# Kernel tuning notes

Hardware: AMD Instinct MI355X
Metric: run time of the kernel (lower is better)

## Reference

```python
import jax, jax.numpy as jnp
import numpy as np

U, I, D, K, B, NNEG = 500000, 500000, 64, 32, 8192, 128
W1, W2, W3, W4 = 1e-6, 1.0, 1e-6, 1.0
NEG_WEIGHT, GAMMA, LAMBDA = 200.0, 1e-4, 2.5


def setup_inputs() -> dict:
    key = jax.random.key(0)
    ks = jax.random.split(key, 14)
    return {
        "users": jax.random.randint(ks[0], (B,), 0, U),
        "pos_items": jax.random.randint(ks[1], (B,), 0, I),
        "neg_items": jax.random.randint(ks[2], (B, NNEG), 0, I),
        "rpkms": jax.random.normal(ks[3], (B,), dtype=jnp.float32),
        "user_emb": jax.random.normal(ks[4], (U, D), dtype=jnp.float32) * 1e-2,
        "item_emb": jax.random.normal(ks[5], (I, D), dtype=jnp.float32) * 1e-2,
        "beta_uD": jax.random.uniform(ks[6], (U,), dtype=jnp.float32),
        "beta_iD": jax.random.uniform(ks[7], (I,), dtype=jnp.float32),
        "ii_neighbor_mat": jax.random.randint(ks[8], (I, K), 0, I),
        "ii_constraint_mat": jax.random.uniform(ks[9], (I, K), dtype=jnp.float32),
        "mse_u_w": jax.random.normal(ks[10], (D, D), dtype=jnp.float32) * 0.05,
        "mse_u_b": jnp.zeros((D,), jnp.float32),
        "mse_i_w": jax.random.normal(ks[11], (D, D), dtype=jnp.float32) * 0.05,
        "mse_i_b": jnp.zeros((D,), jnp.float32),
        "fc1_w1": jax.random.normal(ks[12], (D, 2 * D), dtype=jnp.float32) * 0.05,
        "fc1_b1": jnp.zeros((D,), jnp.float32),
        "fc1_w2": jax.random.normal(ks[13], (1, D), dtype=jnp.float32) * 0.05,
        "fc1_b2": jnp.zeros((1,), jnp.float32),
    }


def reference(users, pos_items, neg_items, rpkms, user_emb, item_emb,
              beta_uD, beta_iD, ii_neighbor_mat, ii_constraint_mat,
              mse_u_w, mse_u_b, mse_i_w, mse_i_b,
              fc1_w1, fc1_b1, fc1_w2, fc1_b2):
    sp = jax.nn.softplus  # -log(sigmoid(x)) == softplus(-x)

    ue = user_emb[users]            # [B, D]
    pe = item_emb[pos_items]        # [B, D]
    ne = item_emb[neg_items]        # [B, N, D]

    # ---- omegas ----
    pos_w = W1 + W2 * beta_uD[users] * beta_iD[pos_items]          # [B]
    neg_w = W3 + W4 * beta_uD[users][:, None] * beta_iD[neg_items]  # [B, N]

    # ---- cal_loss_L (weighted BCE with logits) ----
    pos_scores = jnp.sum(ue * pe, axis=-1)                  # [B]
    neg_scores = jnp.einsum('bd,bnd->bn', ue, ne)           # [B, N]
    pos_loss = pos_w * sp(-pos_scores)                      # label 1
    neg_loss = jnp.mean(neg_w * sp(neg_scores), axis=-1)    # label 0, mean over negs
    loss_L = jnp.mean(pos_loss + neg_loss * NEG_WEIGHT)

    # ---- norm_loss over all learned parameters ----
    params = (user_emb, item_emb, mse_u_w, mse_u_b, mse_i_w, mse_i_b,
              fc1_w1, fc1_b1, fc1_w2, fc1_b2)
    norm = GAMMA * 0.5 * sum(jnp.sum(p * p) for p in params)

    # ---- cal_loss_I: gather item-item neighbors of pos_items ----
    nbr = item_emb[ii_neighbor_mat[pos_items]]              # [B, K, D]
    sim = ii_constraint_mat[pos_items]                      # [B, K]
    loss_I = LAMBDA * jnp.mean(sim * sp(-jnp.einsum('bd,bkd->bk', ue, nbr)))

    # ---- mse_loss ----
    feat_u = ue @ mse_u_w.T + mse_u_b
    feat_i = pe @ mse_i_w.T + mse_i_b
    pred = jnp.sum(feat_u * feat_i, axis=-1)
    mse = jnp.mean((pred - rpkms) ** 2)

    total = loss_L + norm + loss_I + mse
    zero = jnp.float32(0.0)  # torch returns torch.tensor(0.0) as 4th element
    return jnp.stack([total, loss_L, loss_I, zero, mse, norm])
```

## Files before the change

kernel.cpp:

```cpp
#include <hip/hip_runtime.h>
#include <math.h>

#define UU 500000
#define II 500000
#define DD 64
#define KK 32
#define BB 8192
#define NNEG 128

typedef float v4f __attribute__((ext_vector_type(4)));

__device__ __forceinline__ float softplus_f(float x) {
    return fmaxf(x, 0.0f) + log1pf(expf(-fabsf(x)));
}

__device__ __forceinline__ float waveReduceSum(float v) {
#pragma unroll
    for (int off = 32; off > 0; off >>= 1) v += __shfl_xor(v, off, 64);
    return v;
}

__device__ __forceinline__ unsigned int bf16pack2(float lo, float hi) {
    unsigned int ul = __float_as_uint(lo);
    ul += 0x7FFFu + ((ul >> 16) & 1u);
    unsigned int uh = __float_as_uint(hi);
    uh += 0x7FFFu + ((uh >> 16) & 1u);
    return (ul >> 16) | (uh & 0xFFFF0000u);
}

__global__ __launch_bounds__(256) void norm_convert_kernel(
    const float* __restrict__ user_emb, const float* __restrict__ item_emb,
    unsigned int* __restrict__ bfit,
    const float* __restrict__ mse_u_w, const float* __restrict__ mse_u_b,
    const float* __restrict__ mse_i_w, const float* __restrict__ mse_i_b,
    const float* __restrict__ fc1_w1, const float* __restrict__ fc1_b1,
    const float* __restrict__ fc1_w2, const float* __restrict__ fc1_b2,
    float* __restrict__ acc)
{
    const size_t tid = (size_t)blockIdx.x * blockDim.x + threadIdx.x;
    const size_t st  = (size_t)gridDim.x * blockDim.x;
    float s = 0.f;

    {
        const size_t npair = (size_t)II * DD / 8;
        const v4f* it4 = (const v4f*)item_emb;
        uint4* out4 = (uint4*)bfit;
        for (size_t k = tid; k < npair; k += st) {
            v4f a = __builtin_nontemporal_load(&it4[2 * k]);
            v4f b = __builtin_nontemporal_load(&it4[2 * k + 1]);
            s += a.x*a.x + a.y*a.y + a.z*a.z + a.w*a.w;
            s += b.x*b.x + b.y*b.y + b.z*b.z + b.w*b.w;
            uint4 w;
            w.x = bf16pack2(a.x, a.y);
            w.y = bf16pack2(a.z, a.w);
            w.z = bf16pack2(b.x, b.y);
            w.w = bf16pack2(b.z, b.w);
            out4[k] = w;
        }
    }
    {
        const size_t n4 = (size_t)UU * DD / 4;
        const v4f* a = (const v4f*)user_emb;
        for (size_t i = tid; i < n4; i += st) {
            v4f x = __builtin_nontemporal_load(&a[i]);
            s += x.x*x.x + x.y*x.y + x.z*x.z + x.w*x.w;
        }
    }
    for (size_t i = tid; i < (size_t)DD * DD; i += st)
        s += mse_u_w[i] * mse_u_w[i] + mse_i_w[i] * mse_i_w[i];
    for (size_t i = tid; i < (size_t)DD * 2 * DD; i += st)
        s += fc1_w1[i] * fc1_w1[i];
    for (size_t i = tid; i < (size_t)DD; i += st)
        s += mse_u_b[i] * mse_u_b[i] + mse_i_b[i] * mse_i_b[i]
           + fc1_b1[i] * fc1_b1[i] + fc1_w2[i] * fc1_w2[i];
    if (tid == 0) s += fc1_b2[0] * fc1_b2[0];

    s = waveReduceSum(s);
    __shared__ float red[4];
    if ((threadIdx.x & 63) == 0) red[threadIdx.x >> 6] = s;
    __syncthreads();
    if (threadIdx.x == 0)
        atomicAdd(&acc[2], red[0] + red[1] + red[2] + red[3]);
}

__global__ __launch_bounds__(256) void gather_mse_kernel(
    const int* __restrict__ users, const int* __restrict__ pos_items,
    const int* __restrict__ neg_items, const float* __restrict__ rpkms,
    const float* __restrict__ user_emb, const float* __restrict__ item_emb,
    const unsigned int* __restrict__ bfit,
    const float* __restrict__ beta_uD, const float* __restrict__ beta_iD,
    const int* __restrict__ ii_nbr, const float* __restrict__ ii_con,
    const float* __restrict__ mse_u_w, const float* __restrict__ mse_u_b,
    const float* __restrict__ mse_i_w, const float* __restrict__ mse_i_b,
    float* __restrict__ acc)
{
    const int wave = threadIdx.x >> 6;
    const int lane = threadIdx.x & 63;
    const int b = blockIdx.x * 4 + wave;

    const int u_idx = users[b];
    const int p_idx = pos_items[b];
    const float u_reg = user_emb[(size_t)u_idx * DD + lane];
    const float p_reg = item_emb[(size_t)p_idx * DD + lane];
    const float bu = beta_uD[u_idx];

    __shared__ float sU[4][DD];
    __shared__ float sP[4][DD];
    sU[wave][lane] = u_reg;
    sP[wave][lane] = p_reg;

    const int q  = lane & 3;
    const int li = lane >> 2;

    float4 uv[4], pv[4];
#pragma unroll
    for (int j = 0; j < 4; ++j) {
        uv[j] = *(const float4*)&sU[wave][q * 16 + j * 4];
        pv[j] = *(const float4*)&sP[wave][q * 16 + j * 4];
    }

    float accL = 0.f, accI = 0.f, accM = 0.f;

    {
        const float pos_dot = waveReduceSum(u_reg * p_reg);
        if (lane == 0)
            accL += (1e-6f + bu * beta_iD[p_idx]) * softplus_f(-pos_dot);
    }

    const int i0 = neg_items[(size_t)b * NNEG + lane];
    const int i1 = neg_items[(size_t)b * NNEG + 64 + lane];
    const float bn0 = beta_iD[i0];
    const float bn1 = beta_iD[i1];
    int nbv = 0; float simv = 0.f;
    if (lane < KK) {
        nbv  = ii_nbr[(size_t)p_idx * KK + lane];
        simv = ii_con[(size_t)p_idx * KK + lane];
    }

    const float negscale4 = 0.25f * (200.0f / (float)NNEG);

    uint4 rg[3][2];
    float rw[3];

#define PREP(g, slot)                                                          \
    {                                                                          \
        int idx; float w;                                                      \
        if ((g) < 4)      { idx = __shfl(i0, (g) * 16 + li, 64);               \
                            w   = __shfl(bn0, (g) * 16 + li, 64); }            \
        else if ((g) < 8) { idx = __shfl(i1, ((g) - 4) * 16 + li, 64);         \
                            w   = __shfl(bn1, ((g) - 4) * 16 + li, 64); }      \
        else              { idx = __shfl(nbv, ((g) - 8) * 16 + li, 64);        \
                            w   = __shfl(simv, ((g) - 8) * 16 + li, 64); }     \
        const uint4* row = (const uint4*)(bfit + (size_t)idx * (DD / 2));      \
        rg[slot][0] = row[q * 2];                                              \
        rg[slot][1] = row[q * 2 + 1];                                          \
        rw[slot] = w;                                                          \
    }

#define DOT8(wv, ua, ub, d)                                                    \
    {                                                                          \
        d = fmaf(__uint_as_float((wv).x << 16), ua.x, d);                      \
        d = fmaf(__uint_as_float((wv).x & 0xFFFF0000u), ua.y, d);              \
        d = fmaf(__uint_as_float((wv).y << 16), ua.z, d);                      \
        d = fmaf(__uint_as_float((wv).y & 0xFFFF0000u), ua.w, d);              \
        d = fmaf(__uint_as_float((wv).z << 16), ub.x, d);                      \
        d = fmaf(__uint_as_float((wv).z & 0xFFFF0000u), ub.y, d);              \
        d = fmaf(__uint_as_float((wv).w << 16), ub.z, d);                      \
        d = fmaf(__uint_as_float((wv).w & 0xFFFF0000u), ub.w, d);              \
    }

#define CONSUME(g, slot)                                                       \
    {                                                                          \
        float dot = 0.f;                                                       \
        DOT8(rg[slot][0], uv[0], uv[1], dot);                                  \
        DOT8(rg[slot][1], uv[2], uv[3], dot);                                  \
        dot += __shfl_xor(dot, 1, 64);                                         \
        dot += __shfl_xor(dot, 2, 64);                                         \
        if ((g) < 8) accL += negscale4 * (1e-6f + bu * rw[slot]) * softplus_f(dot); \
        else         accI += 0.25f * rw[slot] * softplus_f(-dot);              \
    }

    PREP(0, 0); PREP(1, 1); PREP(2, 2);
    CONSUME(0, 0); PREP(3, 0);
    CONSUME(1, 1); PREP(4, 1);
    CONSUME(2, 2); PREP(5, 2);
    CONSUME(3, 0); PREP(6, 0);
    CONSUME(4, 1); PREP(7, 1);
    CONSUME(5, 2); PREP(8, 2);
    CONSUME(6, 0); PREP(9, 0);
    CONSUME(7, 1);
    CONSUME(8, 2);
    CONSUME(9, 0);
#undef PREP
#undef DOT8
#undef CONSUME

    {
        float pq = 0.f;
#pragma unroll
        for (int g = 0; g < 4; ++g) {
            const int r = g * 16 + li;
            const float* wur = mse_u_w + r * DD + q * 16;
            const float* wir = mse_i_w + r * DD + q * 16;
            float fu = 0.f, fi = 0.f;
#pragma unroll
            for (int j = 0; j < 4; ++j) {
                const float4 a = *(const float4*)(wur + j * 4);
                fu = fmaf(a.x, uv[j].x, fu); fu = fmaf(a.y, uv[j].y, fu);
                fu = fmaf(a.z, uv[j].z, fu); fu = fmaf(a.w, uv[j].w, fu);
                const float4 c = *(const float4*)(wir + j * 4);
                fi = fmaf(c.x, pv[j].x, fi); fi = fmaf(c.y, pv[j].y, fi);
                fi = fmaf(c.z, pv[j].z, fi); fi = fmaf(c.w, pv[j].w, fi);
            }
            fu += __shfl_xor(fu, 1, 64); fu += __shfl_xor(fu, 2, 64);
            fi += __shfl_xor(fi, 1, 64); fi += __shfl_xor(fi, 2, 64);
            fu += mse_u_b[r];
            fi += mse_i_b[r];
            pq += fu * fi;
        }
        const float pred = waveReduceSum(pq) * 0.25f;
        if (lane == 0) {
            const float diff = pred - rpkms[b];
            accM += diff * diff;
        }
    }

    accL = waveReduceSum(accL);
    accI = waveReduceSum(accI);
    __shared__ float redL[4], redI[4], redM[4];
    if (lane == 0) { redL[wave] = accL; redI[wave] = accI; redM[wave] = accM; }
    __syncthreads();
    if (threadIdx.x == 0) {
        atomicAdd(&acc[0], redL[0] + redL[1] + redL[2] + redL[3]);
        atomicAdd(&acc[1], redI[0] + redI[1] + redI[2] + redI[3]);
        atomicAdd(&acc[3], redM[0] + redM[1] + redM[2] + redM[3]);
    }
}

#define NORMB 1024
__global__ __launch_bounds__(256) void fb_fused_kernel(
    const int* __restrict__ users, const int* __restrict__ pos_items,
    const int* __restrict__ neg_items,
    const float* __restrict__ user_emb, const float* __restrict__ item_emb,
    const float* __restrict__ beta_uD, const float* __restrict__ beta_iD,
    const int* __restrict__ ii_nbr, const float* __restrict__ ii_con,
    const float* __restrict__ mse_u_w, const float* __restrict__ mse_u_b,
    const float* __restrict__ mse_i_w, const float* __restrict__ mse_i_b,
    const float* __restrict__ fc1_w1, const float* __restrict__ fc1_b1,
    const float* __restrict__ fc1_w2, const float* __restrict__ fc1_b2,
    float* __restrict__ acc)
{
    const int wave = threadIdx.x >> 6;
    const int lane = threadIdx.x & 63;
    __shared__ float red[4];

    if (blockIdx.x < NORMB) {
        const size_t tid = (size_t)blockIdx.x * blockDim.x + threadIdx.x;
        const size_t st  = (size_t)NORMB * 256;
        const size_t n4  = (size_t)UU * DD / 4;
        float s = 0.f;
        const v4f* a = (const v4f*)user_emb;
        for (size_t i = tid; i < n4; i += st) {
            v4f x = a[i]; s += x.x*x.x + x.y*x.y + x.z*x.z + x.w*x.w;
        }
        const v4f* c = (const v4f*)item_emb;
        for (size_t i = tid; i < n4; i += st) {
            v4f x = c[i]; s += x.x*x.x + x.y*x.y + x.z*x.z + x.w*x.w;
        }
        for (size_t i = tid; i < (size_t)DD * DD; i += st)
            s += mse_u_w[i] * mse_u_w[i] + mse_i_w[i] * mse_i_w[i];
        for (size_t i = tid; i < (size_t)DD * 2 * DD; i += st)
            s += fc1_w1[i] * fc1_w1[i];
        for (size_t i = tid; i < (size_t)DD; i += st)
            s += mse_u_b[i] * mse_u_b[i] + mse_i_b[i] * mse_i_b[i]
               + fc1_b1[i] * fc1_b1[i] + fc1_w2[i] * fc1_w2[i];
        if (tid == 0) s += fc1_b2[0] * fc1_b2[0];
        s = waveReduceSum(s);
        if (lane == 0) red[wave] = s;
        __syncthreads();
        if (threadIdx.x == 0)
            atomicAdd(&acc[2], red[0] + red[1] + red[2] + red[3]);
        return;
    }

    const int b = (blockIdx.x - NORMB) * 4 + wave;
    float accL = 0.f, accI = 0.f;
    const int u_idx = users[b];
    const int p_idx = pos_items[b];
    const float u_reg = user_emb[(size_t)u_idx * DD + lane];
    const float bu = beta_uD[u_idx];
    __shared__ float sU[4][DD];
    sU[wave][lane] = u_reg;
    const int q  = lane & 3;
    const int li = lane >> 2;
    float4 uv[4];
#pragma unroll
    for (int j = 0; j < 4; ++j) uv[j] = *(const float4*)&sU[wave][j * 16 + q * 4];
    {
        const float p = item_emb[(size_t)p_idx * DD + lane];
        const float pos_dot = waveReduceSum(u_reg * p);
        if (lane == 0) accL += (1e-6f + bu * beta_iD[p_idx]) * softplus_f(-pos_dot);
    }
    const int i0 = neg_items[(size_t)b * NNEG + lane];
    const int i1 = neg_items[(size_t)b * NNEG + 64 + lane];
    const float bn0 = beta_iD[i0];
    const float bn1 = beta_iD[i1];
    const float negscale4 = 0.25f * (200.0f / (float)NNEG);
#pragma unroll
    for (int g = 0; g < 2; ++g) {
        const int   srcI = g ? i1 : i0;
        const float srcB = g ? bn1 : bn0;
        float4 vb[4][4]; float bi4[4];
#pragma unroll
        for (int t = 0; t < 4; ++t) {
            const int n = t * 16 + li;
            const int idx = __shfl(srcI, n, 64);
            bi4[t] = __shfl(srcB, n, 64);
            const float* row = item_emb + (size_t)idx * DD + q * 4;
#pragma unroll
            for (int j = 0; j < 4; ++j) vb[t][j] = *(const float4*)(row + j * 16);
        }
#pragma unroll
        for (int t = 0; t < 4; ++t) {
            float dot = 0.f;
#pragma unroll
            for (int j = 0; j < 4; ++j) {
                dot = fmaf(vb[t][j].x, uv[j].x, dot);
                dot = fmaf(vb[t][j].y, uv[j].y, dot);
                dot = fmaf(vb[t][j].z, uv[j].z, dot);
                dot = fmaf(vb[t][j].w, uv[j].w, dot);
            }
            dot += __shfl_xor(dot, 1, 64);
            dot += __shfl_xor(dot, 2, 64);
            accL += negscale4 * (1e-6f + bu * bi4[t]) * softplus_f(dot);
        }
    }
    int nbv = 0; float simv = 0.f;
    if (lane < KK) {
        nbv  = ii_nbr[(size_t)p_idx * KK + lane];
        simv = ii_con[(size_t)p_idx * KK + lane];
    }
    {
        float4 vb[2][4]; float sk2[2];
#pragma unroll
        for (int t = 0; t < 2; ++t) {
            const int n = t * 16 + li;
            const int idx = __shfl(nbv, n, 64);
            sk2[t] = __shfl(simv, n, 64);
            const float* row = item_emb + (size_t)idx * DD + q * 4;
#pragma unroll
            for (int j = 0; j < 4; ++j) vb[t][j] = *(const float4*)(row + j * 16);
        }
#pragma unroll
        for (int t = 0; t < 2; ++t) {
            float dot = 0.f;
#pragma unroll
            for (int j = 0; j < 4; ++j) {
                dot = fmaf(vb[t][j].x, uv[j].x, dot);
                dot = fmaf(vb[t][j].y, uv[j].y, dot);
                dot = fmaf(vb[t][j].z, uv[j].z, dot);
                dot = fmaf(vb[t][j].w, uv[j].w, dot);
            }
            dot += __shfl_xor(dot, 1, 64);
            dot += __shfl_xor(dot, 2, 64);
            accI += 0.25f * sk2[t] * softplus_f(-dot);
        }
    }
    accL = waveReduceSum(accL);
    accI = waveReduceSum(accI);
    __shared__ float redL[4], redI[4];
    if (lane == 0) { redL[wave] = accL; redI[wave] = accI; }
    __syncthreads();
    if (threadIdx.x == 0) {
        atomicAdd(&acc[0], redL[0] + redL[1] + redL[2] + redL[3]);
        atomicAdd(&acc[1], redI[0] + redI[1] + redI[2] + redI[3]);
    }
}

__global__ __launch_bounds__(256) void fb_mse_kernel(
    const int* __restrict__ users, const int* __restrict__ pos_items,
    const float* __restrict__ rpkms,
    const float* __restrict__ user_emb, const float* __restrict__ item_emb,
    const float* __restrict__ mse_u_w, const float* __restrict__ mse_u_b,
    const float* __restrict__ mse_i_w, const float* __restrict__ mse_i_b,
    float* __restrict__ acc)
{
    __shared__ float sWu[DD * (DD + 1)];
    __shared__ float sWi[DD * (DD + 1)];
    __shared__ float sBu[DD], sBi[DD];
    __shared__ float sUe[4][DD], sPe[4][DD];
    for (int i = threadIdx.x; i < DD * DD; i += blockDim.x) {
        const int r = i >> 6, c = i & 63;
        sWu[r * (DD + 1) + c] = mse_u_w[i];
        sWi[r * (DD + 1) + c] = mse_i_w[i];
    }
    if (threadIdx.x < DD) {
        sBu[threadIdx.x] = mse_u_b[threadIdx.x];
        sBi[threadIdx.x] = mse_i_b[threadIdx.x];
    }
    const int wave = threadIdx.x >> 6;
    const int lane = threadIdx.x & 63;
    const int b = blockIdx.x * 4 + wave;
    sUe[wave][lane] = user_emb[(size_t)users[b] * DD + lane];
    sPe[wave][lane] = item_emb[(size_t)pos_items[b] * DD + lane];
    __syncthreads();
    float fu = sBu[lane];
    float fi = sBi[lane];
#pragma unroll 8
    for (int d = 0; d < DD; ++d) {
        fu += sUe[wave][d] * sWu[lane * (DD + 1) + d];
        fi += sPe[wave][d] * sWi[lane * (DD + 1) + d];
    }
    const float pred = waveReduceSum(fu * fi);
    if (lane == 0) {
        const float diff = pred - rpkms[b];
        atomicAdd(&acc[3], diff * diff);
    }
}

__global__ void finalize_kernel(const float* __restrict__ acc, float* __restrict__ out)
{
    if (threadIdx.x == 0) {
        const float loss_L = acc[0] / (float)BB;
        const float loss_I = 2.5f * acc[1] / (float)(BB * KK);
        const float mse    = acc[3] / (float)BB;
        const float norm   = 1e-4f * 0.5f * acc[2];
        const float total  = loss_L + norm + loss_I + mse;
        out[0] = total;
        out[1] = loss_L;
        out[2] = loss_I;
        out[3] = 0.0f;
        out[4] = mse;
        out[5] = norm;
    }
}

extern "C" void kernel_launch(void* const* d_in, const int* in_sizes, int n_in,
                              void* d_out, int out_size, void* d_ws, size_t ws_size,
                              hipStream_t stream)
{
    const int*   users      = (const int*)  d_in[0];
    const int*   pos_items  = (const int*)  d_in[1];
    const int*   neg_items  = (const int*)  d_in[2];
    const float* rpkms      = (const float*)d_in[3];
    const float* user_emb   = (const float*)d_in[4];
    const float* item_emb   = (const float*)d_in[5];
    const float* beta_uD    = (const float*)d_in[6];
    const float* beta_iD    = (const float*)d_in[7];
    const int*   ii_nbr     = (const int*)  d_in[8];
    const float* ii_con     = (const float*)d_in[9];
    const float* mse_u_w    = (const float*)d_in[10];
    const float* mse_u_b    = (const float*)d_in[11];
    const float* mse_i_w    = (const float*)d_in[12];
    const float* mse_i_b    = (const float*)d_in[13];
    const float* fc1_w1     = (const float*)d_in[14];
    const float* fc1_b1     = (const float*)d_in[15];
    const float* fc1_w2     = (const float*)d_in[16];
    const float* fc1_b2     = (const float*)d_in[17];

    float* acc = (float*)d_ws;
    hipMemsetAsync(d_ws, 0, 4 * sizeof(float), stream);

    const size_t bf_bytes = (size_t)II * DD * 2;
    const size_t need = 256 + bf_bytes;

    if (ws_size >= need) {
        unsigned int* bfit = (unsigned int*)((char*)d_ws + 256);
        norm_convert_kernel<<<4096, 256, 0, stream>>>(
            user_emb, item_emb, bfit,
            mse_u_w, mse_u_b, mse_i_w, mse_i_b,
            fc1_w1, fc1_b1, fc1_w2, fc1_b2, acc);
        gather_mse_kernel<<<BB / 4, 256, 0, stream>>>(
            users, pos_items, neg_items, rpkms,
            user_emb, item_emb, bfit, beta_uD, beta_iD,
            ii_nbr, ii_con, mse_u_w, mse_u_b, mse_i_w, mse_i_b, acc);
    } else {
        fb_fused_kernel<<<NORMB + BB / 4, 256, 0, stream>>>(
            users, pos_items, neg_items,
            user_emb, item_emb, beta_uD, beta_iD, ii_nbr, ii_con,
            mse_u_w, mse_u_b, mse_i_w, mse_i_b,
            fc1_w1, fc1_b1, fc1_w2, fc1_b2, acc);
        fb_mse_kernel<<<BB / 4, 256, 0, stream>>>(
            users, pos_items, rpkms, user_emb, item_emb,
            mse_u_w, mse_u_b, mse_i_w, mse_i_b, acc);
    }

    finalize_kernel<<<1, 64, 0, stream>>>(acc, (float*)d_out);
}
```

Before: 477.1 us.

## Fuse user norm reduction and finalize into gather kernel, widen gather prefetch

Moves the user_emb and small-parameter norm reduction from the conversion kernel into the gather kernel, so streaming reads overlap latency-bound random row gathers. Replaces the separate finalize launch with a last-block-done counter that writes the outputs. Restructures the gather to use 8 lanes per bf16 row with 8 rows in flight instead of 4 lanes with 3. This adds an extra atomic counter and per-block grid-stride work, and raises register pressure.

```diff
diff --git a/kernel.cpp b/kernel.cpp
--- a/kernel.cpp
+++ b/kernel.cpp
@@ -28,52 +28,30 @@
     return (ul >> 16) | (uh & 0xFFFF0000u);
 }
 
-__global__ __launch_bounds__(256) void norm_convert_kernel(
-    const float* __restrict__ user_emb, const float* __restrict__ item_emb,
+__global__ __launch_bounds__(256) void item_norm_convert_kernel(
+    const float* __restrict__ item_emb,
     unsigned int* __restrict__ bfit,
-    const float* __restrict__ mse_u_w, const float* __restrict__ mse_u_b,
-    const float* __restrict__ mse_i_w, const float* __restrict__ mse_i_b,
-    const float* __restrict__ fc1_w1, const float* __restrict__ fc1_b1,
-    const float* __restrict__ fc1_w2, const float* __restrict__ fc1_b2,
     float* __restrict__ acc)
 {
     const size_t tid = (size_t)blockIdx.x * blockDim.x + threadIdx.x;
     const size_t st  = (size_t)gridDim.x * blockDim.x;
     float s = 0.f;
 
-    {
-        const size_t npair = (size_t)II * DD / 8;
-        const v4f* it4 = (const v4f*)item_emb;
-        uint4* out4 = (uint4*)bfit;
-        for (size_t k = tid; k < npair; k += st) {
-            v4f a = __builtin_nontemporal_load(&it4[2 * k]);
-            v4f b = __builtin_nontemporal_load(&it4[2 * k + 1]);
-            s += a.x*a.x + a.y*a.y + a.z*a.z + a.w*a.w;
-            s += b.x*b.x + b.y*b.y + b.z*b.z + b.w*b.w;
-            uint4 w;
-            w.x = bf16pack2(a.x, a.y);
-            w.y = bf16pack2(a.z, a.w);
-            w.z = bf16pack2(b.x, b.y);
-            w.w = bf16pack2(b.z, b.w);
-            out4[k] = w;
-        }
-    }
-    {
-        const size_t n4 = (size_t)UU * DD / 4;
-        const v4f* a = (const v4f*)user_emb;
-        for (size_t i = tid; i < n4; i += st) {
-            v4f x = __builtin_nontemporal_load(&a[i]);
-            s += x.x*x.x + x.y*x.y + x.z*x.z + x.w*x.w;
-        }
-    }
-    for (size_t i = tid; i < (size_t)DD * DD; i += st)
-        s += mse_u_w[i] * mse_u_w[i] + mse_i_w[i] * mse_i_w[i];
-    for (size_t i = tid; i < (size_t)DD * 2 * DD; i += st)
-        s += fc1_w1[i] * fc1_w1[i];
-    for (size_t i = tid; i < (size_t)DD; i += st)
-        s += mse_u_b[i] * mse_u_b[i] + mse_i_b[i] * mse_i_b[i]
-           + fc1_b1[i] * fc1_b1[i] + fc1_w2[i] * fc1_w2[i];
-    if (tid == 0) s += fc1_b2[0] * fc1_b2[0];
+    const size_t npair = (size_t)II * DD / 8;
+    const v4f* it4 = (const v4f*)item_emb;
+    uint4* out4 = (uint4*)bfit;
+    for (size_t k = tid; k < npair; k += st) {
+        v4f a = __builtin_nontemporal_load(&it4[2 * k]);
+        v4f b = __builtin_nontemporal_load(&it4[2 * k + 1]);
+        s += a.x*a.x + a.y*a.y + a.z*a.z + a.w*a.w;
+        s += b.x*b.x + b.y*b.y + b.z*b.z + b.w*b.w;
+        uint4 w;
+        w.x = bf16pack2(a.x, a.y);
+        w.y = bf16pack2(a.z, a.w);
+        w.z = bf16pack2(b.x, b.y);
+        w.w = bf16pack2(b.z, b.w);
+        out4[k] = w;
+    }
 
     s = waveReduceSum(s);
     __shared__ float red[4];
@@ -83,7 +61,7 @@
         atomicAdd(&acc[2], red[0] + red[1] + red[2] + red[3]);
 }
 
-__global__ __launch_bounds__(256) void gather_mse_kernel(
+__global__ __launch_bounds__(256) void gather_fused_kernel(
     const int* __restrict__ users, const int* __restrict__ pos_items,
     const int* __restrict__ neg_items, const float* __restrict__ rpkms,
     const float* __restrict__ user_emb, const float* __restrict__ item_emb,
@@ -92,7 +70,10 @@
     const int* __restrict__ ii_nbr, const float* __restrict__ ii_con,
     const float* __restrict__ mse_u_w, const float* __restrict__ mse_u_b,
     const float* __restrict__ mse_i_w, const float* __restrict__ mse_i_b,
-    float* __restrict__ acc)
+    const float* __restrict__ fc1_w1, const float* __restrict__ fc1_b1,
+    const float* __restrict__ fc1_w2, const float* __restrict__ fc1_b2,
+    float* __restrict__ acc, unsigned int* __restrict__ cnt,
+    float* __restrict__ out)
 {
     const int wave = threadIdx.x >> 6;
     const int lane = threadIdx.x & 63;
@@ -109,15 +90,11 @@
     sU[wave][lane] = u_reg;
     sP[wave][lane] = p_reg;
 
-    const int q  = lane & 3;
-    const int li = lane >> 2;
-
-    float4 uv[4], pv[4];
-#pragma unroll
-    for (int j = 0; j < 4; ++j) {
-        uv[j] = *(const float4*)&sU[wave][q * 16 + j * 4];
-        pv[j] = *(const float4*)&sP[wave][q * 16 + j * 4];
-    }
+    const int o  = lane & 7;
+    const int li = lane >> 3;
+
+    float4 uv0 = *(const float4*)&sU[wave][o * 8];
+    float4 uv1 = *(const float4*)&sU[wave][o * 8 + 4];
 
     float accL = 0.f, accI = 0.f, accM = 0.f;
 
@@ -137,80 +114,96 @@
         simv = ii_con[(size_t)p_idx * KK + lane];
     }
 
-    const float negscale4 = 0.25f * (200.0f / (float)NNEG);
-
-    uint4 rg[3][2];
-    float rw[3];
-
-#define PREP(g, slot)                                                          \
+    const float negscale8 = 0.125f * (200.0f / (float)NNEG);
+
+    uint4 rg0, rg1, rg2, rg3, rg4, rg5, rg6, rg7;
+
+#define PREP(g, s)                                                             \
     {                                                                          \
-        int idx; float w;                                                      \
-        if ((g) < 4)      { idx = __shfl(i0, (g) * 16 + li, 64);               \
-                            w   = __shfl(bn0, (g) * 16 + li, 64); }            \
-        else if ((g) < 8) { idx = __shfl(i1, ((g) - 4) * 16 + li, 64);         \
-                            w   = __shfl(bn1, ((g) - 4) * 16 + li, 64); }      \
-        else              { idx = __shfl(nbv, ((g) - 8) * 16 + li, 64);        \
-                            w   = __shfl(simv, ((g) - 8) * 16 + li, 64); }     \
-        const uint4* row = (const uint4*)(bfit + (size_t)idx * (DD / 2));      \
-        rg[slot][0] = row[q * 2];                                              \
-        rg[slot][1] = row[q * 2 + 1];                                          \
-        rw[slot] = w;                                                          \
+        int idx_;                                                              \
+        if ((g) < 8)       idx_ = __shfl(i0, (g) * 8 + li, 64);                \
+        else if ((g) < 16) idx_ = __shfl(i1, ((g) - 8) * 8 + li, 64);          \
+        else               idx_ = __shfl(nbv, ((g) - 16) * 8 + li, 64);        \
+        rg##s = ((const uint4*)(bfit + (size_t)idx_ * (DD / 2)))[o];           \
     }
 
 #define DOT8(wv, ua, ub, d)                                                    \
     {                                                                          \
-        d = fmaf(__uint_as_float((wv).x << 16), ua.x, d);                      \
-        d = fmaf(__uint_as_float((wv).x & 0xFFFF0000u), ua.y, d);              \
-        d = fmaf(__uint_as_float((wv).y << 16), ua.z, d);                      \
-        d = fmaf(__uint_as_float((wv).y & 0xFFFF0000u), ua.w, d);              \
-        d = fmaf(__uint_as_float((wv).z << 16), ub.x, d);                      \
-        d = fmaf(__uint_as_float((wv).z & 0xFFFF0000u), ub.y, d);              \
-        d = fmaf(__uint_as_float((wv).w << 16), ub.z, d);                      \
-        d = fmaf(__uint_as_float((wv).w & 0xFFFF0000u), ub.w, d);              \
-    }
-
-#define CONSUME(g, slot)                                                       \
+        d = fmaf(__uint_as_float((wv).x << 16),          (ua).x, d);           \
+        d = fmaf(__uint_as_float((wv).x & 0xFFFF0000u),  (ua).y, d);           \
+        d = fmaf(__uint_as_float((wv).y << 16),          (ua).z, d);           \
+        d = fmaf(__uint_as_float((wv).y & 0xFFFF0000u),  (ua).w, d);           \
+        d = fmaf(__uint_as_float((wv).z << 16),          (ub).x, d);           \
+        d = fmaf(__uint_as_float((wv).z & 0xFFFF0000u),  (ub).y, d);           \
+        d = fmaf(__uint_as_float((wv).w << 16),          (ub).z, d);           \
+        d = fmaf(__uint_as_float((wv).w & 0xFFFF0000u),  (ub).w, d);           \
+    }
+
+#define CONSUME(g, s)                                                          \
     {                                                                          \
+        float w_;                                                              \
+        if ((g) < 8)       w_ = __shfl(bn0, (g) * 8 + li, 64);                 \
+        else if ((g) < 16) w_ = __shfl(bn1, ((g) - 8) * 8 + li, 64);           \
+        else               w_ = __shfl(simv, ((g) - 16) * 8 + li, 64);         \
         float dot = 0.f;                                                       \
-        DOT8(rg[slot][0], uv[0], uv[1], dot);                                  \
-        DOT8(rg[slot][1], uv[2], uv[3], dot);                                  \
+        DOT8(rg##s, uv0, uv1, dot);                                            \
         dot += __shfl_xor(dot, 1, 64);                                         \
         dot += __shfl_xor(dot, 2, 64);                                         \
-        if ((g) < 8) accL += negscale4 * (1e-6f + bu * rw[slot]) * softplus_f(dot); \
-        else         accI += 0.25f * rw[slot] * softplus_f(-dot);              \
-    }
-
-    PREP(0, 0); PREP(1, 1); PREP(2, 2);
-    CONSUME(0, 0); PREP(3, 0);
-    CONSUME(1, 1); PREP(4, 1);
-    CONSUME(2, 2); PREP(5, 2);
-    CONSUME(3, 0); PREP(6, 0);
-    CONSUME(4, 1); PREP(7, 1);
-    CONSUME(5, 2); PREP(8, 2);
-    CONSUME(6, 0); PREP(9, 0);
-    CONSUME(7, 1);
-    CONSUME(8, 2);
-    CONSUME(9, 0);
+        dot += __shfl_xor(dot, 4, 64);                                         \
+        if ((g) < 16) accL += negscale8 * (1e-6f + bu * w_) * softplus_f(dot); \
+        else          accI += 0.125f * w_ * softplus_f(-dot);                  \
+    }
+
+    PREP(0, 0); PREP(1, 1); PREP(2, 2); PREP(3, 3);
+    PREP(4, 4); PREP(5, 5); PREP(6, 6); PREP(7, 7);
+    CONSUME(0, 0);  PREP(8, 0);
+    CONSUME(1, 1);  PREP(9, 1);
+    CONSUME(2, 2);  PREP(10, 2);
+    CONSUME(3, 3);  PREP(11, 3);
+    CONSUME(4, 4);  PREP(12, 4);
+    CONSUME(5, 5);  PREP(13, 5);
+    CONSUME(6, 6);  PREP(14, 6);
+    CONSUME(7, 7);  PREP(15, 7);
+    CONSUME(8, 0);  PREP(16, 0);
+    CONSUME(9, 1);  PREP(17, 1);
+    CONSUME(10, 2); PREP(18, 2);
+    CONSUME(11, 3); PREP(19, 3);
+    CONSUME(12, 4);
+    CONSUME(13, 5);
+    CONSUME(14, 6);
+    CONSUME(15, 7);
+    CONSUME(16, 0);
+    CONSUME(17, 1);
+    CONSUME(18, 2);
+    CONSUME(19, 3);
 #undef PREP
 #undef DOT8
 #undef CONSUME
 
     {
+        const int q4  = lane & 3;
+        const int li4 = lane >> 2;
+        float4 uv4[4], pv4[4];
+#pragma unroll
+        for (int j = 0; j < 4; ++j) {
+            uv4[j] = *(const float4*)&sU[wave][q4 * 16 + j * 4];
+            pv4[j] = *(const float4*)&sP[wave][q4 * 16 + j * 4];
+        }
         float pq = 0.f;
 #pragma unroll
         for (int g = 0; g < 4; ++g) {
-            const int r = g * 16 + li;
-            const float* wur = mse_u_w + r * DD + q * 16;
-            const float* wir = mse_i_w + r * DD + q * 16;
+            const int r = g * 16 + li4;
+            const float* wur = mse_u_w + r * DD + q4 * 16;
+            const float* wir = mse_i_w + r * DD + q4 * 16;
             float fu = 0.f, fi = 0.f;
 #pragma unroll
             for (int j = 0; j < 4; ++j) {
                 const float4 a = *(const float4*)(wur + j * 4);
-                fu = fmaf(a.x, uv[j].x, fu); fu = fmaf(a.y, uv[j].y, fu);
-                fu = fmaf(a.z, uv[j].z, fu); fu = fmaf(a.w, uv[j].w, fu);
+                fu = fmaf(a.x, uv4[j].x, fu); fu = fmaf(a.y, uv4[j].y, fu);
+                fu = fmaf(a.z, uv4[j].z, fu); fu = fmaf(a.w, uv4[j].w, fu);
                 const float4 c = *(const float4*)(wir + j * 4);
-                fi = fmaf(c.x, pv[j].x, fi); fi = fmaf(c.y, pv[j].y, fi);
-                fi = fmaf(c.z, pv[j].z, fi); fi = fmaf(c.w, pv[j].w, fi);
+                fi = fmaf(c.x, pv4[j].x, fi); fi = fmaf(c.y, pv4[j].y, fi);
+                fi = fmaf(c.z, pv4[j].z, fi); fi = fmaf(c.w, pv4[j].w, fi);
             }
             fu += __shfl_xor(fu, 1, 64); fu += __shfl_xor(fu, 2, 64);
             fi += __shfl_xor(fi, 1, 64); fi += __shfl_xor(fi, 2, 64);
@@ -225,15 +218,55 @@
         }
     }
 
+    float sN = 0.f;
+    {
+        const size_t tid = (size_t)blockIdx.x * blockDim.x + threadIdx.x;
+        const size_t st  = (size_t)gridDim.x * blockDim.x;
+        const size_t n4  = (size_t)UU * DD / 4;
+        const v4f* a = (const v4f*)user_emb;
+        for (size_t i = tid; i < n4; i += st) {
+            v4f x = __builtin_nontemporal_load(&a[i]);
+            sN += x.x*x.x + x.y*x.y + x.z*x.z + x.w*x.w;
+        }
+        for (size_t i = tid; i < (size_t)DD * DD; i += st)
+            sN += mse_u_w[i] * mse_u_w[i] + mse_i_w[i] * mse_i_w[i];
+        for (size_t i = tid; i < (size_t)DD * 2 * DD; i += st)
+            sN += fc1_w1[i] * fc1_w1[i];
+        for (size_t i = tid; i < (size_t)DD; i += st)
+            sN += mse_u_b[i] * mse_u_b[i] + mse_i_b[i] * mse_i_b[i]
+                + fc1_b1[i] * fc1_b1[i] + fc1_w2[i] * fc1_w2[i];
+        if (tid == 0) sN += fc1_b2[0] * fc1_b2[0];
+    }
+
     accL = waveReduceSum(accL);
     accI = waveReduceSum(accI);
-    __shared__ float redL[4], redI[4], redM[4];
-    if (lane == 0) { redL[wave] = accL; redI[wave] = accI; redM[wave] = accM; }
+    sN   = waveReduceSum(sN);
+    __shared__ float redL[4], redI[4], redM[4], redN[4];
+    if (lane == 0) { redL[wave] = accL; redI[wave] = accI; redM[wave] = accM; redN[wave] = sN; }
     __syncthreads();
     if (threadIdx.x == 0) {
         atomicAdd(&acc[0], redL[0] + redL[1] + redL[2] + redL[3]);
         atomicAdd(&acc[1], redI[0] + redI[1] + redI[2] + redI[3]);
+        atomicAdd(&acc[2], redN[0] + redN[1] + redN[2] + redN[3]);
         atomicAdd(&acc[3], redM[0] + redM[1] + redM[2] + redM[3]);
+        __threadfence();
+        const unsigned int t = atomicAdd(cnt, 1u);
+        if (t == (unsigned int)(gridDim.x - 1)) {
+            const float sL  = atomicAdd(&acc[0], 0.0f);
+            const float sI  = atomicAdd(&acc[1], 0.0f);
+            const float sNo = atomicAdd(&acc[2], 0.0f);
+            const float sM  = atomicAdd(&acc[3], 0.0f);
+            const float loss_L = sL / (float)BB;
+            const float loss_I = 2.5f * sI / (float)(BB * KK);
+            const float mse    = sM / (float)BB;
+            const float nrm    = 1e-4f * 0.5f * sNo;
+            out[0] = loss_L + nrm + loss_I + mse;
+            out[1] = loss_L;
+            out[2] = loss_I;
+            out[3] = 0.0f;
+            out[4] = mse;
+            out[5] = nrm;
+        }
     }
 }
 
@@ -459,21 +492,21 @@
     const float* fc1_b2     = (const float*)d_in[17];
 
     float* acc = (float*)d_ws;
-    hipMemsetAsync(d_ws, 0, 4 * sizeof(float), stream);
+    unsigned int* cnt = (unsigned int*)d_ws + 4;
+    hipMemsetAsync(d_ws, 0, 8 * sizeof(float), stream);
 
     const size_t bf_bytes = (size_t)II * DD * 2;
     const size_t need = 256 + bf_bytes;
 
     if (ws_size >= need) {
         unsigned int* bfit = (unsigned int*)((char*)d_ws + 256);
-        norm_convert_kernel<<<4096, 256, 0, stream>>>(
-            user_emb, item_emb, bfit,
-            mse_u_w, mse_u_b, mse_i_w, mse_i_b,
-            fc1_w1, fc1_b1, fc1_w2, fc1_b2, acc);
-        gather_mse_kernel<<<BB / 4, 256, 0, stream>>>(
+        item_norm_convert_kernel<<<4096, 256, 0, stream>>>(item_emb, bfit, acc);
+        gather_fused_kernel<<<BB / 4, 256, 0, stream>>>(
             users, pos_items, neg_items, rpkms,
             user_emb, item_emb, bfit, beta_uD, beta_iD,
-            ii_nbr, ii_con, mse_u_w, mse_u_b, mse_i_w, mse_i_b, acc);
+            ii_nbr, ii_con, mse_u_w, mse_u_b, mse_i_w, mse_i_b,
+            fc1_w1, fc1_b1, fc1_w2, fc1_b2,
+            acc, cnt, (float*)d_out);
     } else {
         fb_fused_kernel<<<NORMB + BB / 4, 256, 0, stream>>>(
             users, pos_items, neg_items,
@@ -483,7 +516,6 @@
         fb_mse_kernel<<<BB / 4, 256, 0, stream>>>(
             users, pos_items, rpkms, user_emb, item_emb,
             mse_u_w, mse_u_b, mse_i_w, mse_i_b, acc);
-    }
-
-    finalize_kernel<<<1, 64, 0, stream>>>(acc, (float*)d_out);
-}
+        finalize_kernel<<<1, 64, 0, stream>>>(acc, (float*)d_out);
+    }
+}
```

New measurement: 554.6 us. 1.16x slower.

## Split each batch row across two waves and fold finalize into last block

Applied to the files above, without the earlier changes.

Each batch row's ten gather groups of negatives and neighbors are now divided between two waves instead of one. Each block handles two rows, so twice as many blocks are launched, with a launch-bounds occupancy hint. Only the first wave loads the positive item and computes the MSE term. The separate finalize kernel is removed: a global atomic counter lets the last block compute the output, trading a threadfence and extra atomics per block for one fewer launch and more memory-level parallelism in the latency-bound gather.

```diff
diff --git a/kernel.cpp b/kernel.cpp
--- a/kernel.cpp
+++ b/kernel.cpp
@@ -83,7 +83,7 @@
         atomicAdd(&acc[2], red[0] + red[1] + red[2] + red[3]);
 }
 
-__global__ __launch_bounds__(256) void gather_mse_kernel(
+__global__ __launch_bounds__(256, 8) void gather_split_kernel(
     const int* __restrict__ users, const int* __restrict__ pos_items,
     const int* __restrict__ neg_items, const float* __restrict__ rpkms,
     const float* __restrict__ user_emb, const float* __restrict__ item_emb,
@@ -92,36 +92,37 @@
     const int* __restrict__ ii_nbr, const float* __restrict__ ii_con,
     const float* __restrict__ mse_u_w, const float* __restrict__ mse_u_b,
     const float* __restrict__ mse_i_w, const float* __restrict__ mse_i_b,
-    float* __restrict__ acc)
+    float* __restrict__ acc, unsigned int* __restrict__ cnt,
+    float* __restrict__ out)
 {
     const int wave = threadIdx.x >> 6;
     const int lane = threadIdx.x & 63;
-    const int b = blockIdx.x * 4 + wave;
+    const int pair = wave >> 1;
+    const int half = wave & 1;
+    const int b = blockIdx.x * 2 + pair;
 
     const int u_idx = users[b];
     const int p_idx = pos_items[b];
     const float u_reg = user_emb[(size_t)u_idx * DD + lane];
-    const float p_reg = item_emb[(size_t)p_idx * DD + lane];
     const float bu = beta_uD[u_idx];
 
     __shared__ float sU[4][DD];
-    __shared__ float sP[4][DD];
+    __shared__ float sP[2][DD];
     sU[wave][lane] = u_reg;
-    sP[wave][lane] = p_reg;
 
     const int q  = lane & 3;
     const int li = lane >> 2;
 
-    float4 uv[4], pv[4];
-#pragma unroll
-    for (int j = 0; j < 4; ++j) {
+    float4 uv[4];
+#pragma unroll
+    for (int j = 0; j < 4; ++j)
         uv[j] = *(const float4*)&sU[wave][q * 16 + j * 4];
-        pv[j] = *(const float4*)&sP[wave][q * 16 + j * 4];
-    }
 
     float accL = 0.f, accI = 0.f, accM = 0.f;
 
-    {
+    if (half == 0) {
+        const float p_reg = item_emb[(size_t)p_idx * DD + lane];
+        sP[pair][lane] = p_reg;
         const float pos_dot = waveReduceSum(u_reg * p_reg);
         if (lane == 0)
             accL += (1e-6f + bu * beta_iD[p_idx]) * softplus_f(-pos_dot);
@@ -180,22 +181,30 @@
         else         accI += 0.25f * rw[slot] * softplus_f(-dot);              \
     }
 
-    PREP(0, 0); PREP(1, 1); PREP(2, 2);
-    CONSUME(0, 0); PREP(3, 0);
-    CONSUME(1, 1); PREP(4, 1);
-    CONSUME(2, 2); PREP(5, 2);
-    CONSUME(3, 0); PREP(6, 0);
-    CONSUME(4, 1); PREP(7, 1);
-    CONSUME(5, 2); PREP(8, 2);
-    CONSUME(6, 0); PREP(9, 0);
-    CONSUME(7, 1);
-    CONSUME(8, 2);
-    CONSUME(9, 0);
+    if (half == 0) {
+        PREP(0, 0); PREP(1, 1); PREP(2, 2);
+        CONSUME(0, 0); PREP(3, 0);
+        CONSUME(1, 1); PREP(4, 1);
+        CONSUME(2, 2);
+        CONSUME(3, 0);
+        CONSUME(4, 1);
+    } else {
+        PREP(5, 0); PREP(6, 1); PREP(7, 2);
+        CONSUME(5, 0); PREP(8, 0);
+        CONSUME(6, 1); PREP(9, 1);
+        CONSUME(7, 2);
+        CONSUME(8, 0);
+        CONSUME(9, 1);
+    }
 #undef PREP
 #undef DOT8
 #undef CONSUME
 
-    {
+    if (half == 0) {
+        float4 pv[4];
+#pragma unroll
+        for (int j = 0; j < 4; ++j)
+            pv[j] = *(const float4*)&sP[pair][q * 16 + j * 4];
         float pq = 0.f;
 #pragma unroll
         for (int g = 0; g < 4; ++g) {
@@ -234,6 +243,24 @@
         atomicAdd(&acc[0], redL[0] + redL[1] + redL[2] + redL[3]);
         atomicAdd(&acc[1], redI[0] + redI[1] + redI[2] + redI[3]);
         atomicAdd(&acc[3], redM[0] + redM[1] + redM[2] + redM[3]);
+        __threadfence();
+        const unsigned int t = atomicAdd(cnt, 1u);
+        if (t == (unsigned int)(gridDim.x - 1)) {
+            const float sL  = atomicAdd(&acc[0], 0.0f);
+            const float sI  = atomicAdd(&acc[1], 0.0f);
+            const float sNo = atomicAdd(&acc[2], 0.0f);
+            const float sM  = atomicAdd(&acc[3], 0.0f);
+            const float loss_L = sL / (float)BB;
+            const float loss_I = 2.5f * sI / (float)(BB * KK);
+            const float mse    = sM / (float)BB;
+            const float nrm    = 1e-4f * 0.5f * sNo;
+            out[0] = loss_L + nrm + loss_I + mse;
+            out[1] = loss_L;
+            out[2] = loss_I;
+            out[3] = 0.0f;
+            out[4] = mse;
+            out[5] = nrm;
+        }
     }
 }
 
@@ -459,7 +486,8 @@
     const float* fc1_b2     = (const float*)d_in[17];
 
     float* acc = (float*)d_ws;
-    hipMemsetAsync(d_ws, 0, 4 * sizeof(float), stream);
+    unsigned int* cnt = (unsigned int*)d_ws + 4;
+    hipMemsetAsync(d_ws, 0, 8 * sizeof(float), stream);
 
     const size_t bf_bytes = (size_t)II * DD * 2;
     const size_t need = 256 + bf_bytes;
@@ -470,10 +498,11 @@
             user_emb, item_emb, bfit,
             mse_u_w, mse_u_b, mse_i_w, mse_i_b,
             fc1_w1, fc1_b1, fc1_w2, fc1_b2, acc);
-        gather_mse_kernel<<<BB / 4, 256, 0, stream>>>(
+        gather_split_kernel<<<BB / 2, 256, 0, stream>>>(
             users, pos_items, neg_items, rpkms,
             user_emb, item_emb, bfit, beta_uD, beta_iD,
-            ii_nbr, ii_con, mse_u_w, mse_u_b, mse_i_w, mse_i_b, acc);
+            ii_nbr, ii_con, mse_u_w, mse_u_b, mse_i_w, mse_i_b,
+            acc, cnt, (float*)d_out);
     } else {
         fb_fused_kernel<<<NORMB + BB / 4, 256, 0, stream>>>(
             users, pos_items, neg_items,
@@ -483,7 +512,6 @@
         fb_mse_kernel<<<BB / 4, 256, 0, stream>>>(
             users, pos_items, rpkms, user_emb, item_emb,
             mse_u_w, mse_u_b, mse_i_w, mse_i_b, acc);
-    }
-
-    finalize_kernel<<<1, 64, 0, stream>>>(acc, (float*)d_out);
-}
+        finalize_kernel<<<1, 64, 0, stream>>>(acc, (float*)d_out);
+    }
+}
```

Measured after the change: 619.6 us. +29.9%, slower.
